# Performance work log

Hardware: AMD Instinct MI355X
Metric: run time of the kernel (lower is better)

## Reference

```python
import jax, jax.numpy as jnp
import numpy as np

DIM = 2048
NUM_HEADS = 32
NUM_KV_HEADS = 8
HEAD_DIM = DIM // NUM_HEADS           # 64
KV_REPEAT = NUM_HEADS // NUM_KV_HEADS  # 4
KV_DIM = HEAD_DIM * NUM_KV_HEADS      # 512
THRESHOLD = 0.05


def _init_weight(key, out_f, in_f):
    # kaiming_uniform(a=sqrt(5)) ~ U(-1/sqrt(in_f), 1/sqrt(in_f))
    bound = 1.0 / np.sqrt(in_f)
    return jax.random.uniform(key, (out_f, in_f), jnp.float32, -bound, bound)


def ternarize_ste(w):
    scale = jnp.maximum(jnp.abs(w).mean(), 1e-6)
    t = jnp.where(w > THRESHOLD * scale, 1.0,
                  jnp.where(w < -THRESHOLD * scale, -1.0, 0.0))
    return w + jax.lax.stop_gradient(t - w)


def setup_inputs() -> dict:
    key = jax.random.key(0)
    kx, kq, kk, kv, ko = jax.random.split(key, 5)
    x = jax.random.normal(kx, (2, 2048, DIM), jnp.float32)
    wq = _init_weight(kq, DIM, DIM)
    wk = _init_weight(kk, KV_DIM, DIM)
    wv = _init_weight(kv, KV_DIM, DIM)
    wo = _init_weight(ko, DIM, DIM)
    return {"x": x, "wq": wq, "wk": wk, "wv": wv, "wo": wo}


def reference(x, wq, wk, wv, wo):
    b, s, _ = x.shape
    g, r, d = NUM_KV_HEADS, KV_REPEAT, HEAD_DIM
    q = x @ ternarize_ste(wq).T   # [b,s,dim]
    k = x @ ternarize_ste(wk).T   # [b,s,kv_dim]
    v = x @ ternarize_ste(wv).T   # [b,s,kv_dim]
    # group heads as (kv_group g, repeat r) to avoid physically expanding KV
    q = q.reshape(b, s, g, r, d)
    k = k.reshape(b, s, g, d)
    v = v.reshape(b, s, g, d)
    att = jnp.einsum('bqgrd,bkgd->bgrqk', q, k) / np.sqrt(d).astype(jnp.float32)
    causal = jnp.tril(jnp.ones((s, s), dtype=bool))  # [q,k] keep lower tri
    att = jnp.where(causal, att, -jnp.inf)
    probs = jax.nn.softmax(att, axis=-1)
    out = jnp.einsum('bgrqk,bkgd->bqgrd', probs, v).reshape(b, s, DIM)
    return out @ ternarize_ste(wo).T
```

## Files before the change

### kernel.cpp

```cpp
#include <hip/hip_runtime.h>
#include <hip/hip_bf16.h>
#include <stdint.h>

#define DIMN 2048
#define KVD  512
#define NH   32
#define BATCH 2
#define SEQ  2048
#define ROWS (BATCH*SEQ)
#define NT   (SEQ/64)

typedef __attribute__((ext_vector_type(4))) float f32x4;
typedef __attribute__((ext_vector_type(8))) short bf16x8;

__device__ __forceinline__ float bf2f(short s){
  union{uint32_t u;float f;} v; v.u=((uint32_t)(uint16_t)s)<<16; return v.f;
}
__device__ __forceinline__ short f2bf(float f){
  union{float f;uint32_t u;} v; v.f=f;
  uint32_t r=(v.u + 0x7fffu + ((v.u>>16)&1u))>>16; return (short)r;
}
__device__ __forceinline__ f32x4 mfma16(bf16x8 a, bf16x8 b, f32x4 c){
  return __builtin_amdgcn_mfma_f32_16x16x32_bf16(a,b,c,0,0,0);
}
__device__ __forceinline__ short ternbf(float v, float thr){
  return v > thr ? (short)0x3F80 : (v < -thr ? (short)0xBF80 : (short)0);
}

__global__ void k_abssum4(const float* __restrict__ w0, const float* __restrict__ w1,
                          const float* __restrict__ w2, const float* __restrict__ w3,
                          float* __restrict__ partial){
  __shared__ float red[256];
  const float* ptrs[4] = {w0, w1, w2, w3};
  const int ns[4] = {DIMN*DIMN, KVD*DIMN, KVD*DIMN, DIMN*DIMN};
  const int wi = blockIdx.y;
  const float* w = ptrs[wi];
  const int n = ns[wi];
  float s = 0.f;
  for (int i = blockIdx.x*256 + threadIdx.x; i < n; i += 256*gridDim.x) s += fabsf(w[i]);
  red[threadIdx.x] = s; __syncthreads();
  for (int o = 128; o > 0; o >>= 1){
    if (threadIdx.x < o) red[threadIdx.x] += red[threadIdx.x+o];
    __syncthreads();
  }
  if (threadIdx.x == 0) partial[wi*256 + blockIdx.x] = red[0];
}

__global__ void k_scales(const float* __restrict__ partial, float* __restrict__ scales){
  __shared__ float red[256];
  int t = threadIdx.x;
  const int counts[4] = {DIMN*DIMN, KVD*DIMN, KVD*DIMN, DIMN*DIMN};
  for (int wi = 0; wi < 4; wi++){
    red[t] = partial[wi*256 + t]; __syncthreads();
    for (int o = 128; o > 0; o >>= 1){
      if (t < o) red[t] += red[t+o];
      __syncthreads();
    }
    if (t == 0){
      float mean = red[0] / (float)counts[wi];
      scales[wi] = 0.05f * fmaxf(mean, 1e-6f);
    }
    __syncthreads();
  }
}

__global__ void k_prep_x(const float* __restrict__ x, short* __restrict__ hi,
                         short* __restrict__ lo){
  long i = ((long)blockIdx.x*256 + threadIdx.x)*8;
  f32x4 a = *(const f32x4*)(x+i);
  f32x4 b = *(const f32x4*)(x+i+4);
  bf16x8 h, l;
  #pragma unroll
  for (int j = 0; j < 4; j++){
    short p = f2bf(a[j]); h[j]   = p; l[j]   = f2bf(a[j]-bf2f(p));
    short q = f2bf(b[j]); h[4+j] = q; l[4+j] = f2bf(b[j]-bf2f(q));
  }
  *(bf16x8*)(hi+i) = h;
  *(bf16x8*)(lo+i) = l;
}

__global__ void k_tern4(const float* __restrict__ w0, const float* __restrict__ w1,
                        const float* __restrict__ w2, const float* __restrict__ w3,
                        short* __restrict__ o0, short* __restrict__ o1,
                        short* __restrict__ o2, short* __restrict__ o3,
                        const float* __restrict__ scales){
  const float* ws[4] = {w0, w1, w2, w3};
  short* os[4] = {o0, o1, o2, o3};
  const int ns[4] = {DIMN*DIMN, KVD*DIMN, KVD*DIMN, DIMN*DIMN};
  const int wi = blockIdx.y;
  long i = ((long)blockIdx.x*256 + threadIdx.x)*8;
  if (i >= ns[wi]) return;
  const float thr = scales[wi];
  const float* w = ws[wi];
  f32x4 a = *(const f32x4*)(w+i);
  f32x4 b = *(const f32x4*)(w+i+4);
  bf16x8 t;
  #pragma unroll
  for (int j = 0; j < 4; j++){
    t[j]   = ternbf(a[j], thr);
    t[4+j] = ternbf(b[j], thr);
  }
  *(bf16x8*)(os[wi]+i) = t;
}

template<int SPLITA, int SPLITB, int OUTF32>
__device__ __forceinline__ void gemm_core(
    const short* __restrict__ Ahg, const short* __restrict__ Alg,
    const short* __restrict__ Bg,  const short* __restrict__ Blg,
    float* __restrict__ Of, short* __restrict__ Oh, short* __restrict__ Ol,
    bool writelo, int N, int K, int bn, int bm,
    short (*AhS)[72], short (*AlS)[72], short (*BsS)[72], short (*BlS)[72]){
  const int tid = threadIdx.x, lane = tid & 63, w = tid >> 6;
  const int wr = w >> 1, wc = w & 1;
  const int la = lane & 15, kg = lane >> 4;
  const int srow = tid >> 1, sc = (tid & 1) * 32;
  f32x4 acc[4][4] = {};
  for (int k0 = 0; k0 < K; k0 += 64){
    {
      const short* ap = Ahg + (long)(bm+srow)*K + k0 + sc;
      #pragma unroll
      for (int i = 0; i < 4; i++)
        *(bf16x8*)&AhS[srow][sc+i*8] = *(const bf16x8*)(ap + i*8);
    }
    if constexpr (SPLITA){
      const short* alp = Alg + (long)(bm+srow)*K + k0 + sc;
      #pragma unroll
      for (int i = 0; i < 4; i++)
        *(bf16x8*)&AlS[srow][sc+i*8] = *(const bf16x8*)(alp + i*8);
    }
    {
      const short* bp = Bg + (long)(bn+srow)*K + k0 + sc;
      #pragma unroll
      for (int i = 0; i < 4; i++)
        *(bf16x8*)&BsS[srow][sc+i*8] = *(const bf16x8*)(bp + i*8);
    }
    if constexpr (SPLITB){
      const short* blp = Blg + (long)(bn+srow)*K + k0 + sc;
      #pragma unroll
      for (int i = 0; i < 4; i++)
        *(bf16x8*)&BlS[srow][sc+i*8] = *(const bf16x8*)(blp + i*8);
    }
    __syncthreads();
    #pragma unroll
    for (int ks = 0; ks < 2; ks++){
      bf16x8 af[4], bfr[4];
      #pragma unroll
      for (int mi = 0; mi < 4; mi++)
        af[mi] = *(bf16x8*)&AhS[wr*64 + mi*16 + la][ks*32 + kg*8];
      #pragma unroll
      for (int ni = 0; ni < 4; ni++)
        bfr[ni] = *(bf16x8*)&BsS[wc*64 + ni*16 + la][ks*32 + kg*8];
      #pragma unroll
      for (int mi = 0; mi < 4; mi++)
        #pragma unroll
        for (int ni = 0; ni < 4; ni++)
          acc[mi][ni] = mfma16(af[mi], bfr[ni], acc[mi][ni]);
      if constexpr (SPLITA){
        bf16x8 alf[4];
        #pragma unroll
        for (int mi = 0; mi < 4; mi++)
          alf[mi] = *(bf16x8*)&AlS[wr*64 + mi*16 + la][ks*32 + kg*8];
        #pragma unroll
        for (int mi = 0; mi < 4; mi++)
          #pragma unroll
          for (int ni = 0; ni < 4; ni++)
            acc[mi][ni] = mfma16(alf[mi], bfr[ni], acc[mi][ni]);
      }
      if constexpr (SPLITB){
        bf16x8 blf[4];
        #pragma unroll
        for (int ni = 0; ni < 4; ni++)
          blf[ni] = *(bf16x8*)&BlS[wc*64 + ni*16 + la][ks*32 + kg*8];
        #pragma unroll
        for (int mi = 0; mi < 4; mi++)
          #pragma unroll
          for (int ni = 0; ni < 4; ni++)
            acc[mi][ni] = mfma16(af[mi], blf[ni], acc[mi][ni]);
      }
    }
    __syncthreads();
  }
  #pragma unroll
  for (int mi = 0; mi < 4; mi++)
    #pragma unroll
    for (int ni = 0; ni < 4; ni++)
      #pragma unroll
      for (int rr = 0; rr < 4; rr++){
        long row = bm + wr*64 + mi*16 + kg*4 + rr;
        long col = bn + wc*64 + ni*16 + la;
        float v = acc[mi][ni][rr];
        if constexpr (OUTF32){
          Of[row*(long)N + col] = v;
        } else {
          short hb = f2bf(v);
          Oh[row*(long)N + col] = hb;
          if (writelo)
            Ol[row*(long)N + col] = f2bf(v - bf2f(hb));
        }
      }
}

__global__ __launch_bounds__(256) void k_gemm_q(
    const short* __restrict__ Ahg, const short* __restrict__ Alg,
    const short* __restrict__ Bg, short* __restrict__ Oh, short* __restrict__ Ol,
    int N, int K){
  __shared__ short S0[128][72];
  __shared__ short S1[128][72];
  __shared__ short S2[128][72];
  gemm_core<1,0,0>(Ahg, Alg, Bg, nullptr, nullptr, Oh, Ol, true, N, K,
                   blockIdx.x*128, blockIdx.y*128, S0, S1, S2, nullptr);
}

__global__ __launch_bounds__(256) void k_gemm_kvt(
    const short* __restrict__ xhi, const short* __restrict__ xlo,
    const short* __restrict__ wkT, const short* __restrict__ wvT,
    short* __restrict__ KOh, short* __restrict__ KOl, short* __restrict__ VT,
    int K){
  __shared__ short S0[128][72];
  __shared__ short S1[128][72];
  __shared__ short S2[128][72];
  if (blockIdx.z == 0){
    gemm_core<1,0,0>(xhi, xlo, wkT, nullptr, nullptr, KOh, KOl, true, KVD, K,
                     blockIdx.x*128, blockIdx.y*128, S0, S1, S2, nullptr);
  } else {
    gemm_core<0,1,0>(wvT, nullptr, xhi, xlo, nullptr, VT, nullptr, false, ROWS, K,
                     blockIdx.y*128, blockIdx.x*128, S0, nullptr, S1, S2);
  }
}

__global__ __launch_bounds__(256) void k_gemm_o(
    const short* __restrict__ Ahg, const short* __restrict__ Bg,
    float* __restrict__ Of, int N, int K){
  __shared__ short S0[128][72];
  __shared__ short S2[128][72];
  gemm_core<0,0,1>(Ahg, nullptr, Bg, nullptr, Of, nullptr, nullptr, false, N, K,
                   blockIdx.x*128, blockIdx.y*128, S0, nullptr, S2, nullptr);
}

__global__ __launch_bounds__(256) void k_attn(
    const short* __restrict__ qhi, const short* __restrict__ qlo,
    const short* __restrict__ khi, const short* __restrict__ klo,
    const short* __restrict__ vT, short* __restrict__ attout){
  __shared__ short Kh[64][72];
  __shared__ short Kl[64][72];
  __shared__ short Vt[64][72];
  __shared__ short P[64][72];
  const int qp = blockIdx.x, h = blockIdx.y, b = blockIdx.z;
  const int g = h >> 2;
  const int tid = threadIdx.x, w = tid >> 6, lane = tid & 63;
  const int la = lane & 15, kg = lane >> 4;
  const int trow = tid >> 2, tcol = (tid & 3) * 16;

  for (int phase = 0; phase < 2; phase++){
    const int qt = phase ? (NT - 1 - qp) : qp;
    const int qbase = qt*64;

    bf16x8 qh[2], ql[2];
    {
      long qrow = (long)(b*SEQ + qbase + w*16 + la);
      #pragma unroll
      for (int ks = 0; ks < 2; ks++){
        long off = qrow*DIMN + h*64 + ks*32 + kg*8;
        qh[ks] = *(const bf16x8*)(qhi + off);
        ql[ks] = *(const bf16x8*)(qlo + off);
      }
    }
    f32x4 Oacc[4] = {};
    float m[4], l[4];
    #pragma unroll
    for (int r = 0; r < 4; r++){ m[r] = -INFINITY; l[r] = 0.f; }

    for (int kt = 0; kt <= qt; kt++){
      __syncthreads();
      {
        const short* ksrc  = khi + (long)(b*SEQ + kt*64 + trow)*KVD + g*64 + tcol;
        const short* klsrc = klo + (long)(b*SEQ + kt*64 + trow)*KVD + g*64 + tcol;
        const short* vsrc  = vT  + (long)(g*64 + trow)*ROWS + b*SEQ + kt*64 + tcol;
        *(bf16x8*)&Kh[trow][tcol]   = *(const bf16x8*)ksrc;
        *(bf16x8*)&Kh[trow][tcol+8] = *(const bf16x8*)(ksrc + 8);
        *(bf16x8*)&Kl[trow][tcol]   = *(const bf16x8*)klsrc;
        *(bf16x8*)&Kl[trow][tcol+8] = *(const bf16x8*)(klsrc + 8);
        *(bf16x8*)&Vt[trow][tcol]   = *(const bf16x8*)vsrc;
        *(bf16x8*)&Vt[trow][tcol+8] = *(const bf16x8*)(vsrc + 8);
      }
      __syncthreads();

      f32x4 s[4];
      __builtin_amdgcn_s_setprio(1);
      #pragma unroll
      for (int ni = 0; ni < 4; ni++){
        f32x4 a = {0.f,0.f,0.f,0.f};
        #pragma unroll
        for (int ks = 0; ks < 2; ks++){
          bf16x8 kh = *(bf16x8*)&Kh[ni*16 + la][ks*32 + kg*8];
          bf16x8 kl = *(bf16x8*)&Kl[ni*16 + la][ks*32 + kg*8];
          a = mfma16(qh[ks], kh, a);
          a = mfma16(ql[ks], kh, a);
          a = mfma16(qh[ks], kl, a);
        }
        s[ni] = a;
      }
      __builtin_amdgcn_s_setprio(0);

      const bool lastTile = (kt == qt);
      #pragma unroll
      for (int ni = 0; ni < 4; ni++)
        #pragma unroll
        for (int r = 0; r < 4; r++){
          float v = s[ni][r] * 0.125f;
          if (lastTile){
            int kc = kt*64 + ni*16 + la;
            int qr = qbase + w*16 + kg*4 + r;
            if (kc > qr) v = -INFINITY;
          }
          s[ni][r] = v;
        }

      float ef[4];
      #pragma unroll
      for (int r = 0; r < 4; r++){
        float v = fmaxf(fmaxf(s[0][r], s[1][r]), fmaxf(s[2][r], s[3][r]));
        for (int o = 1; o < 16; o <<= 1) v = fmaxf(v, __shfl_xor(v, o, 64));
        float mn = fmaxf(m[r], v);
        ef[r] = __expf(m[r] - mn);
        m[r] = mn;
      }
      #pragma unroll
      for (int r = 0; r < 4; r++){
        float rs = 0.f;
        #pragma unroll
        for (int ni = 0; ni < 4; ni++){
          float p = __expf(s[ni][r] - m[r]);
          s[ni][r] = p;
          rs += p;
        }
        for (int o = 1; o < 16; o <<= 1) rs += __shfl_xor(rs, o, 64);
        l[r] = l[r]*ef[r] + rs;
      }
      #pragma unroll
      for (int d = 0; d < 4; d++)
        #pragma unroll
        for (int r = 0; r < 4; r++) Oacc[d][r] *= ef[r];

      #pragma unroll
      for (int ni = 0; ni < 4; ni++)
        #pragma unroll
        for (int r = 0; r < 4; r++)
          P[w*16 + kg*4 + r][ni*16 + la] = f2bf(s[ni][r]);

      __builtin_amdgcn_s_setprio(1);
      #pragma unroll
      for (int ks = 0; ks < 2; ks++){
        bf16x8 pa = *(bf16x8*)&P[w*16 + la][ks*32 + kg*8];
        #pragma unroll
        for (int d = 0; d < 4; d++){
          bf16x8 vb = *(bf16x8*)&Vt[d*16 + la][ks*32 + kg*8];
          Oacc[d] = mfma16(pa, vb, Oacc[d]);
        }
      }
      __builtin_amdgcn_s_setprio(0);
    }

    #pragma unroll
    for (int d = 0; d < 4; d++)
      #pragma unroll
      for (int r = 0; r < 4; r++){
        float v = Oacc[d][r] / l[r];
        long row = (long)(b*SEQ + qbase + w*16 + kg*4 + r);
        attout[row*DIMN + h*64 + d*16 + la] = f2bf(v);
      }
    __syncthreads();
  }
}

extern "C" void kernel_launch(void* const* d_in, const int* in_sizes, int n_in,
                              void* d_out, int out_size, void* d_ws, size_t ws_size,
                              hipStream_t stream){
  const float* x  = (const float*)d_in[0];
  const float* wq = (const float*)d_in[1];
  const float* wk = (const float*)d_in[2];
  const float* wv = (const float*)d_in[3];
  const float* wo = (const float*)d_in[4];
  float* out = (float*)d_out;
  char* ws = (char*)d_ws;

  const size_t SZ_QD = (size_t)ROWS*DIMN*2;
  const size_t SZ_KD = (size_t)ROWS*KVD*2;
  const size_t SZ_WQ = (size_t)DIMN*DIMN*2;
  const size_t SZ_WK = (size_t)KVD*DIMN*2;
  const size_t NEED = 65536 + 2*SZ_QD + 2*SZ_WQ + 2*SZ_WK + 2*SZ_QD + 3*SZ_KD;
  if (ws_size < NEED) return;

  float* scales   = (float*)ws;
  float* partials = (float*)(ws + 1024);
  size_t off = 65536;
  auto alloc = [&](size_t bytes)->char*{
    char* p = ws + off; off += (bytes + 255) & ~(size_t)255; return p;
  };
  short* xhi = (short*)alloc(SZ_QD);
  short* xlo = (short*)alloc(SZ_QD);
  short* wqT = (short*)alloc(SZ_WQ);
  short* wkT = (short*)alloc(SZ_WK);
  short* wvT = (short*)alloc(SZ_WK);
  short* woT = (short*)alloc(SZ_WQ);
  short* qhib = (short*)alloc(SZ_QD);
  short* qlob = (short*)alloc(SZ_QD);
  short* khib = (short*)alloc(SZ_KD);
  short* klob = (short*)alloc(SZ_KD);
  short* vTb  = (short*)alloc(SZ_KD);
  short* atto = xhi;

  {
    dim3 g(256, 4);
    k_abssum4<<<g,256,0,stream>>>(wq, wk, wv, wo, partials);
  }
  k_scales<<<1,256,0,stream>>>(partials, scales);

  {
    dim3 g(2048, 4);
    k_tern4<<<g,256,0,stream>>>(wq, wk, wv, wo, wqT, wkT, wvT, woT, scales);
  }
  k_prep_x<<<4096,256,0,stream>>>(x, xhi, xlo);

  {
    dim3 g(DIMN/128, ROWS/128);
    k_gemm_q<<<g,256,0,stream>>>(xhi, xlo, wqT, qhib, qlob, DIMN, DIMN);
  }
  {
    dim3 g(KVD/128, ROWS/128, 2);
    k_gemm_kvt<<<g,256,0,stream>>>(xhi, xlo, wkT, wvT, khib, klob, vTb, DIMN);
  }

  {
    dim3 g(NT/2, NH, BATCH);
    k_attn<<<g,256,0,stream>>>(qhib, qlob, khib, klob, vTb, atto);
  }

  {
    dim3 g(DIMN/128, ROWS/128);
    k_gemm_o<<<g,256,0,stream>>>(atto, woT, out, DIMN, DIMN);
  }
}
```

Measured before the change: 490.7 us.

## Use direct global-to-LDS loads in GEMMs and lazy-rescale exp2 softmax in attention

GEMM tile staging now uses global_load_lds to copy 16-byte chunks straight into unpadded LDS, dropping the register round trip, and the separate A-lo/B-lo buffers merge into one shared lo buffer. In attention, the scale is folded into a log2 factor so softmax can use exp2f, and the running max and accumulators are rescaled only when some row's max grows by more than 8. Attention LDS padding drops from 72 to 68 and f2bf switches to the HIP intrinsic. Unpadded 64-wide GEMM tiles may add LDS bank conflicts on the fragment reads, and the lazy rescale lets probabilities reach up to 2^8 before renormalising.

```diff
diff --git a/kernel.cpp b/kernel.cpp
--- a/kernel.cpp
+++ b/kernel.cpp
@@ -16,15 +16,20 @@
 __device__ __forceinline__ float bf2f(short s){
   union{uint32_t u;float f;} v; v.u=((uint32_t)(uint16_t)s)<<16; return v.f;
 }
-__device__ __forceinline__ short f2bf(float f){
-  union{float f;uint32_t u;} v; v.f=f;
-  uint32_t r=(v.u + 0x7fffu + ((v.u>>16)&1u))>>16; return (short)r;
+__device__ __forceinline__ short f2bf_rn(float f){
+  __hip_bfloat16 h = __float2bfloat16(f);
+  short s; __builtin_memcpy(&s, &h, 2); return s;
 }
 __device__ __forceinline__ f32x4 mfma16(bf16x8 a, bf16x8 b, f32x4 c){
   return __builtin_amdgcn_mfma_f32_16x16x32_bf16(a,b,c,0,0,0);
 }
 __device__ __forceinline__ short ternbf(float v, float thr){
   return v > thr ? (short)0x3F80 : (v < -thr ? (short)0xBF80 : (short)0);
+}
+__device__ __forceinline__ void gload16(const short* g, short* l){
+  __builtin_amdgcn_global_load_lds(
+      (const __attribute__((address_space(1))) uint32_t*)g,
+      (__attribute__((address_space(3))) uint32_t*)l, 16, 0, 0);
 }
 
 __global__ void k_abssum4(const float* __restrict__ w0, const float* __restrict__ w1,
@@ -72,8 +77,8 @@
   bf16x8 h, l;
   #pragma unroll
   for (int j = 0; j < 4; j++){
-    short p = f2bf(a[j]); h[j]   = p; l[j]   = f2bf(a[j]-bf2f(p));
-    short q = f2bf(b[j]); h[4+j] = q; l[4+j] = f2bf(b[j]-bf2f(q));
+    short p = f2bf_rn(a[j]); h[j]   = p; l[j]   = f2bf_rn(a[j]-bf2f(p));
+    short q = f2bf_rn(b[j]); h[4+j] = q; l[4+j] = f2bf_rn(b[j]-bf2f(q));
   }
   *(bf16x8*)(hi+i) = h;
   *(bf16x8*)(lo+i) = l;
@@ -105,40 +110,39 @@
 
 template<int SPLITA, int SPLITB, int OUTF32>
 __device__ __forceinline__ void gemm_core(
-    const short* __restrict__ Ahg, const short* __restrict__ Alg,
-    const short* __restrict__ Bg,  const short* __restrict__ Blg,
+    const short* __restrict__ Ahg, const short* __restrict__ Xlg,
+    const short* __restrict__ Bg,
     float* __restrict__ Of, short* __restrict__ Oh, short* __restrict__ Ol,
     bool writelo, int N, int K, int bn, int bm,
-    short (*AhS)[72], short (*AlS)[72], short (*BsS)[72], short (*BlS)[72]){
+    short (*AhS)[64], short (*XlS)[64], short (*BsS)[64]){
   const int tid = threadIdx.x, lane = tid & 63, w = tid >> 6;
   const int wr = w >> 1, wc = w & 1;
   const int la = lane & 15, kg = lane >> 4;
-  const int srow = tid >> 1, sc = (tid & 1) * 32;
+  const int xrb = SPLITA ? bm : bn;
   f32x4 acc[4][4] = {};
   for (int k0 = 0; k0 < K; k0 += 64){
-    {
-      const short* ap = Ahg + (long)(bm+srow)*K + k0 + sc;
-      #pragma unroll
-      for (int i = 0; i < 4; i++)
-        *(bf16x8*)&AhS[srow][sc+i*8] = *(const bf16x8*)(ap + i*8);
-    }
-    if constexpr (SPLITA){
-      const short* alp = Alg + (long)(bm+srow)*K + k0 + sc;
-      #pragma unroll
-      for (int i = 0; i < 4; i++)
-        *(bf16x8*)&AlS[srow][sc+i*8] = *(const bf16x8*)(alp + i*8);
-    }
-    {
-      const short* bp = Bg + (long)(bn+srow)*K + k0 + sc;
-      #pragma unroll
-      for (int i = 0; i < 4; i++)
-        *(bf16x8*)&BsS[srow][sc+i*8] = *(const bf16x8*)(bp + i*8);
-    }
-    if constexpr (SPLITB){
-      const short* blp = Blg + (long)(bn+srow)*K + k0 + sc;
-      #pragma unroll
-      for (int i = 0; i < 4; i++)
-        *(bf16x8*)&BlS[srow][sc+i*8] = *(const bf16x8*)(blp + i*8);
+    #pragma unroll
+    for (int j = 0; j < 4; j++){
+      const int flat = (w*4 + j)*64 + lane;
+      const int row = flat >> 3, c16 = (flat & 7)*8;
+      short* lb = &AhS[0][0] + (w*4 + j)*512;
+      gload16(Ahg + (long)(bm+row)*K + k0 + c16, lb);
+    }
+    if constexpr (SPLITA || SPLITB){
+      #pragma unroll
+      for (int j = 0; j < 4; j++){
+        const int flat = (w*4 + j)*64 + lane;
+        const int row = flat >> 3, c16 = (flat & 7)*8;
+        short* lb = &XlS[0][0] + (w*4 + j)*512;
+        gload16(Xlg + (long)(xrb+row)*K + k0 + c16, lb);
+      }
+    }
+    #pragma unroll
+    for (int j = 0; j < 4; j++){
+      const int flat = (w*4 + j)*64 + lane;
+      const int row = flat >> 3, c16 = (flat & 7)*8;
+      short* lb = &BsS[0][0] + (w*4 + j)*512;
+      gload16(Bg + (long)(bn+row)*K + k0 + c16, lb);
     }
     __syncthreads();
     #pragma unroll
@@ -159,7 +163,7 @@
         bf16x8 alf[4];
         #pragma unroll
         for (int mi = 0; mi < 4; mi++)
-          alf[mi] = *(bf16x8*)&AlS[wr*64 + mi*16 + la][ks*32 + kg*8];
+          alf[mi] = *(bf16x8*)&XlS[wr*64 + mi*16 + la][ks*32 + kg*8];
         #pragma unroll
         for (int mi = 0; mi < 4; mi++)
           #pragma unroll
@@ -170,7 +174,7 @@
         bf16x8 blf[4];
         #pragma unroll
         for (int ni = 0; ni < 4; ni++)
-          blf[ni] = *(bf16x8*)&BlS[wc*64 + ni*16 + la][ks*32 + kg*8];
+          blf[ni] = *(bf16x8*)&XlS[wc*64 + ni*16 + la][ks*32 + kg*8];
         #pragma unroll
         for (int mi = 0; mi < 4; mi++)
           #pragma unroll
@@ -192,10 +196,10 @@
         if constexpr (OUTF32){
           Of[row*(long)N + col] = v;
         } else {
-          short hb = f2bf(v);
+          short hb = f2bf_rn(v);
           Oh[row*(long)N + col] = hb;
           if (writelo)
-            Ol[row*(long)N + col] = f2bf(v - bf2f(hb));
+            Ol[row*(long)N + col] = f2bf_rn(v - bf2f(hb));
         }
       }
 }
@@ -204,11 +208,11 @@
     const short* __restrict__ Ahg, const short* __restrict__ Alg,
     const short* __restrict__ Bg, short* __restrict__ Oh, short* __restrict__ Ol,
     int N, int K){
-  __shared__ short S0[128][72];
-  __shared__ short S1[128][72];
-  __shared__ short S2[128][72];
-  gemm_core<1,0,0>(Ahg, Alg, Bg, nullptr, nullptr, Oh, Ol, true, N, K,
-                   blockIdx.x*128, blockIdx.y*128, S0, S1, S2, nullptr);
+  __shared__ short S0[128][64];
+  __shared__ short S1[128][64];
+  __shared__ short S2[128][64];
+  gemm_core<1,0,0>(Ahg, Alg, Bg, nullptr, Oh, Ol, true, N, K,
+                   blockIdx.x*128, blockIdx.y*128, S0, S1, S2);
 }
 
 __global__ __launch_bounds__(256) void k_gemm_kvt(
@@ -216,35 +220,36 @@
     const short* __restrict__ wkT, const short* __restrict__ wvT,
     short* __restrict__ KOh, short* __restrict__ KOl, short* __restrict__ VT,
     int K){
-  __shared__ short S0[128][72];
-  __shared__ short S1[128][72];
-  __shared__ short S2[128][72];
+  __shared__ short S0[128][64];
+  __shared__ short S1[128][64];
+  __shared__ short S2[128][64];
   if (blockIdx.z == 0){
-    gemm_core<1,0,0>(xhi, xlo, wkT, nullptr, nullptr, KOh, KOl, true, KVD, K,
-                     blockIdx.x*128, blockIdx.y*128, S0, S1, S2, nullptr);
+    gemm_core<1,0,0>(xhi, xlo, wkT, nullptr, KOh, KOl, true, KVD, K,
+                     blockIdx.x*128, blockIdx.y*128, S0, S1, S2);
   } else {
-    gemm_core<0,1,0>(wvT, nullptr, xhi, xlo, nullptr, VT, nullptr, false, ROWS, K,
-                     blockIdx.y*128, blockIdx.x*128, S0, nullptr, S1, S2);
+    gemm_core<0,1,0>(wvT, xlo, xhi, nullptr, VT, nullptr, false, ROWS, K,
+                     blockIdx.y*128, blockIdx.x*128, S0, S1, S2);
   }
 }
 
 __global__ __launch_bounds__(256) void k_gemm_o(
     const short* __restrict__ Ahg, const short* __restrict__ Bg,
     float* __restrict__ Of, int N, int K){
-  __shared__ short S0[128][72];
-  __shared__ short S2[128][72];
-  gemm_core<0,0,1>(Ahg, nullptr, Bg, nullptr, Of, nullptr, nullptr, false, N, K,
-                   blockIdx.x*128, blockIdx.y*128, S0, nullptr, S2, nullptr);
+  __shared__ short S0[128][64];
+  __shared__ short S2[128][64];
+  gemm_core<0,0,1>(Ahg, nullptr, Bg, Of, nullptr, nullptr, false, N, K,
+                   blockIdx.x*128, blockIdx.y*128, S0, nullptr, S2);
 }
 
 __global__ __launch_bounds__(256) void k_attn(
     const short* __restrict__ qhi, const short* __restrict__ qlo,
     const short* __restrict__ khi, const short* __restrict__ klo,
     const short* __restrict__ vT, short* __restrict__ attout){
-  __shared__ short Kh[64][72];
-  __shared__ short Kl[64][72];
-  __shared__ short Vt[64][72];
-  __shared__ short P[64][72];
+  __shared__ short Kh[64][68];
+  __shared__ short Kl[64][68];
+  __shared__ short Vt[64][68];
+  __shared__ short P[64][68];
+  const float SC = 0.125f * 1.44269504f;
   const int qp = blockIdx.x, h = blockIdx.y, b = blockIdx.z;
   const int g = h >> 2;
   const int tid = threadIdx.x, w = tid >> 6, lane = tid & 63;
@@ -307,7 +312,7 @@
       for (int ni = 0; ni < 4; ni++)
         #pragma unroll
         for (int r = 0; r < 4; r++){
-          float v = s[ni][r] * 0.125f;
+          float v = s[ni][r] * SC;
           if (lastTile){
             int kc = kt*64 + ni*16 + la;
             int qr = qbase + w*16 + kg*4 + r;
@@ -316,37 +321,44 @@
           s[ni][r] = v;
         }
 
-      float ef[4];
+      float pm[4];
       #pragma unroll
       for (int r = 0; r < 4; r++){
         float v = fmaxf(fmaxf(s[0][r], s[1][r]), fmaxf(s[2][r], s[3][r]));
         for (int o = 1; o < 16; o <<= 1) v = fmaxf(v, __shfl_xor(v, o, 64));
-        float mn = fmaxf(m[r], v);
-        ef[r] = __expf(m[r] - mn);
-        m[r] = mn;
+        pm[r] = v;
+      }
+      float gr = -INFINITY;
+      #pragma unroll
+      for (int r = 0; r < 4; r++) gr = fmaxf(gr, pm[r] - m[r]);
+      if (!__all(gr <= 8.0f)){
+        #pragma unroll
+        for (int r = 0; r < 4; r++){
+          float mn = fmaxf(m[r], pm[r]);
+          float ef = exp2f(m[r] - mn);
+          m[r] = mn; l[r] *= ef;
+          #pragma unroll
+          for (int d = 0; d < 4; d++) Oacc[d][r] *= ef;
+        }
       }
       #pragma unroll
       for (int r = 0; r < 4; r++){
         float rs = 0.f;
         #pragma unroll
         for (int ni = 0; ni < 4; ni++){
-          float p = __expf(s[ni][r] - m[r]);
+          float p = exp2f(s[ni][r] - m[r]);
           s[ni][r] = p;
           rs += p;
         }
         for (int o = 1; o < 16; o <<= 1) rs += __shfl_xor(rs, o, 64);
-        l[r] = l[r]*ef[r] + rs;
-      }
-      #pragma unroll
-      for (int d = 0; d < 4; d++)
-        #pragma unroll
-        for (int r = 0; r < 4; r++) Oacc[d][r] *= ef[r];
+        l[r] += rs;
+      }
 
       #pragma unroll
       for (int ni = 0; ni < 4; ni++)
         #pragma unroll
         for (int r = 0; r < 4; r++)
-          P[w*16 + kg*4 + r][ni*16 + la] = f2bf(s[ni][r]);
+          P[w*16 + kg*4 + r][ni*16 + la] = f2bf_rn(s[ni][r]);
 
       __builtin_amdgcn_s_setprio(1);
       #pragma unroll
@@ -367,7 +379,7 @@
       for (int r = 0; r < 4; r++){
         float v = Oacc[d][r] / l[r];
         long row = (long)(b*SEQ + qbase + w*16 + kg*4 + r);
-        attout[row*DIMN + h*64 + d*16 + la] = f2bf(v);
+        attout[row*DIMN + h*64 + d*16 + la] = f2bf_rn(v);
       }
     __syncthreads();
   }
```

New measurement: 513.3 us. 1.05x slower.
